# Optimization experiments

Hardware: AMD Instinct MI355X
Metric: run time of the kernel (lower is better)

Reference implementation:

```python
import jax, jax.numpy as jnp
import numpy as np

B_, D_, L_, N_ = 2, 1536, 2048, 16


def setup_inputs() -> dict:
    key = jax.random.key(0)
    ks = jax.random.split(key, 8)
    x = jax.random.normal(ks[0], (B_, D_, L_), dtype=jnp.float32)
    delta = jax.random.normal(ks[1], (B_, D_, L_), dtype=jnp.float32)
    # A negative (as in Mamba, A = -exp(A_log)) so the recurrence is stable
    A = -(jax.random.uniform(ks[2], (D_, N_), dtype=jnp.float32) + 0.5)
    B = jax.random.normal(ks[3], (B_, N_, L_), dtype=jnp.float32)
    C = jax.random.normal(ks[4], (B_, N_, L_), dtype=jnp.float32)
    D = jax.random.normal(ks[5], (D_,), dtype=jnp.float32)
    z = jax.random.normal(ks[6], (B_, D_, L_), dtype=jnp.float32)
    delta_bias = jax.random.normal(ks[7], (D_,), dtype=jnp.float32)
    return {"x": x, "delta": delta, "A": A, "B": B, "C": C,
            "D": D, "z": z, "delta_bias": delta_bias}


def reference(x, delta, A, B, C, D, z, delta_bias):
    # delta_softplus=True path with delta_bias, variable B (bnl) and C (bnl)
    delta = jax.nn.softplus(delta + delta_bias[None, :, None])      # (b,d,l)
    deltaA = jnp.exp(jnp.einsum('bdl,dn->bdln', delta, A))          # (b,d,l,n)
    deltaB_x = jnp.einsum('bdl,bnl,bdl->bdln', delta, B, x)         # (b,d,l,n)

    # scan over the sequence axis: h = deltaA_t * h + deltaB_x_t; y = h @ C_t
    dA_t = jnp.transpose(deltaA, (2, 0, 1, 3))     # (l,b,d,n)
    dBx_t = jnp.transpose(deltaB_x, (2, 0, 1, 3))  # (l,b,d,n)
    C_t = jnp.transpose(C, (2, 0, 1))              # (l,b,n)

    def step(h, inp):
        dA_i, dBx_i, C_i = inp
        h = dA_i * h + dBx_i                       # (b,d,n)
        y = jnp.einsum('bdn,bn->bd', h, C_i)       # (b,d)
        return h, y

    h0 = jnp.zeros((x.shape[0], A.shape[0], A.shape[1]), dtype=jnp.float32)
    _, ys = jax.lax.scan(step, h0, (dA_t, dBx_t, C_t))  # ys: (l,b,d)
    y = jnp.transpose(ys, (1, 2, 0))                    # (b,d,l)

    out = y + x * D[None, :, None]                      # D skip connection
    out = out * (z * jax.nn.sigmoid(z))                 # SiLU gate
    return out
```

## Files before the change

kernel.cpp:

```cpp
#include <hip/hip_runtime.h>
#include <math.h>

#define B_  2
#define D_  1536
#define L_  2048
#define N_  16
#define NH  8
#define LC  128
#define NCHUNK (L_ / LC)
#define NCH (B_ * D_)
#define LOG2E 1.4426950408889634f
#define LN2   0.6931471805599453f

typedef float f4 __attribute__((ext_vector_type(4)));
typedef float f8 __attribute__((ext_vector_type(8)));

__device__ __forceinline__ float exp2f_(float v) { return __builtin_amdgcn_exp2f(v); }
__device__ __forceinline__ float log2f_(float v) { return __builtin_amdgcn_logf(v); }
__device__ __forceinline__ float rcpf_(float v)  { return __builtin_amdgcn_rcpf(v); }

__device__ __forceinline__ float softplus_f(float v) {
    float t = exp2f_(v * LOG2E);
    float r = LN2 * log2f_(1.0f + t);
    return (v > 20.0f) ? v : r;
}
__device__ __forceinline__ f8 splat8(float v) { f8 r = {v,v,v,v,v,v,v,v}; return r; }
__device__ __forceinline__ f8 exp2v8(f8 a) {
    f8 r;
    r[0]=exp2f_(a[0]); r[1]=exp2f_(a[1]); r[2]=exp2f_(a[2]); r[3]=exp2f_(a[3]);
    r[4]=exp2f_(a[4]); r[5]=exp2f_(a[5]); r[6]=exp2f_(a[6]); r[7]=exp2f_(a[7]);
    return r;
}
__device__ __forceinline__ float dot8(f8 a, f8 b) {
    float p0 = fmaf(a[0], b[0], a[1]*b[1]);
    float p1 = fmaf(a[2], b[2], a[3]*b[3]);
    float p2 = fmaf(a[4], b[4], a[5]*b[5]);
    float p3 = fmaf(a[6], b[6], a[7]*b[7]);
    return (p0 + p1) + (p2 + p3);
}

#define DPP_ROW_SHR(N) (0x110 + (N))
#define DPP_ROW_BCAST15 0x142
#define DPP_WAVE_SHR1   0x138
template<int CTRL, int RMASK>
__device__ __forceinline__ float updpp(float old, float v) {
    return __int_as_float(__builtin_amdgcn_update_dpp(
        __float_as_int(old), __float_as_int(v), CTRL, RMASK, 0xF, false));
}

__global__ __launch_bounds__(64, 3)
void ssm_scan_kernel(const float* __restrict__ x,
                     const float* __restrict__ delta,
                     const float* __restrict__ A,
                     const float* __restrict__ Bm,
                     const float* __restrict__ Cm,
                     const float* __restrict__ Dv,
                     const float* __restrict__ z,
                     const float* __restrict__ dbias,
                     float* __restrict__ out)
{
    const int lane = threadIdx.x;
    const int s    = lane & 31;
    const int g    = lane >> 5;
    const int ch   = blockIdx.x;
    const int b    = ch / D_;
    const int d    = ch - b * D_;

    const float bias = dbias[d];
    const float Dd   = Dv[d];

    const float* Ab = A + d * N_ + NH * g;
    f8 A2v;
    A2v[0]=Ab[0]*LOG2E; A2v[1]=Ab[1]*LOG2E; A2v[2]=Ab[2]*LOG2E; A2v[3]=Ab[3]*LOG2E;
    A2v[4]=Ab[4]*LOG2E; A2v[5]=Ab[5]*LOG2E; A2v[6]=Ab[6]*LOG2E; A2v[7]=Ab[7]*LOG2E;

    const float* Bp = Bm + (size_t)b * (N_ * L_) + (size_t)(NH * g) * L_;
    const float* Cp = Cm + (size_t)b * (N_ * L_) + (size_t)(NH * g) * L_;
    const size_t chbase = (size_t)ch * L_;

    f8 carry = splat8(0.0f);

    for (int c = 0; c < NCHUNK; ++c) {
        const int off = c * LC + s * 4;

        f4 dv = *(const f4*)(delta + chbase + off);
        f4 xv = *(const f4*)(x     + chbase + off);
        f4 zv = *(const f4*)(z     + chbase + off);
#define LD_BC(i) f4 Bv##i = *(const f4*)(Bp + i * L_ + off); \
                 f4 Cv##i = *(const f4*)(Cp + i * L_ + off);
        LD_BC(0) LD_BC(1) LD_BC(2) LD_BC(3) LD_BC(4) LD_BC(5) LD_BC(6) LD_BC(7)

        float dt0 = softplus_f(dv.x + bias);
        float dt1 = softplus_f(dv.y + bias);
        float dt2 = softplus_f(dv.z + bias);
        float dt3 = softplus_f(dv.w + bias);
        float u0 = dt0 * xv.x, u1 = dt1 * xv.y, u2 = dt2 * xv.z, u3 = dt3 * xv.w;
        float dtsum = (dt0 + dt1) + (dt2 + dt3);

        f8 e0 = exp2v8(splat8(dt0) * A2v);
        f8 e1 = exp2v8(splat8(dt1) * A2v);
        f8 e2 = exp2v8(splat8(dt2) * A2v);
        f8 e3 = exp2v8(splat8(dt3) * A2v);
        f8 P  = exp2v8(splat8(dtsum) * A2v);

        f8 tB0 = {Bv0.x,Bv1.x,Bv2.x,Bv3.x,Bv4.x,Bv5.x,Bv6.x,Bv7.x};
        f8 tB1 = {Bv0.y,Bv1.y,Bv2.y,Bv3.y,Bv4.y,Bv5.y,Bv6.y,Bv7.y};
        f8 tB2 = {Bv0.z,Bv1.z,Bv2.z,Bv3.z,Bv4.z,Bv5.z,Bv6.z,Bv7.z};
        f8 tB3 = {Bv0.w,Bv1.w,Bv2.w,Bv3.w,Bv4.w,Bv5.w,Bv6.w,Bv7.w};
        f8 uB0 = splat8(u0) * tB0;
        f8 uB1 = splat8(u1) * tB1;
        f8 uB2 = splat8(u2) * tB2;
        f8 uB3 = splat8(u3) * tB3;
        f8 SC0 = {Cv0.x,Cv1.x,Cv2.x,Cv3.x,Cv4.x,Cv5.x,Cv6.x,Cv7.x};
        f8 SC1 = {Cv0.y,Cv1.y,Cv2.y,Cv3.y,Cv4.y,Cv5.y,Cv6.y,Cv7.y};
        f8 SC2 = {Cv0.z,Cv1.z,Cv2.z,Cv3.z,Cv4.z,Cv5.z,Cv6.z,Cv7.z};
        f8 SC3 = {Cv0.w,Cv1.w,Cv2.w,Cv3.w,Cv4.w,Cv5.w,Cv6.w,Cv7.w};

        f8 S = uB0;
        S = e1 * S + uB1;
        S = e2 * S + uB2;
        S = e3 * S + uB3;

#define SCAN_STEP(CTRL, RMASK) \
        { \
            _Pragma("unroll") \
            for (int i = 0; i < NH; ++i) { \
                float Pp = updpp<CTRL, RMASK>(1.0f, P[i]); \
                float Sp = updpp<CTRL, RMASK>(0.0f, S[i]); \
                S[i] = fmaf(Sp, P[i], S[i]);    \
                P[i] = P[i] * Pp; \
            } \
        }
        SCAN_STEP(DPP_ROW_SHR(1), 0xF)
        SCAN_STEP(DPP_ROW_SHR(2), 0xF)
        SCAN_STEP(DPP_ROW_SHR(4), 0xF)
        SCAN_STEP(DPP_ROW_SHR(8), 0xF)
        SCAN_STEP(DPP_ROW_BCAST15, 0xA)

        f8 h;
#pragma unroll
        for (int i = 0; i < NH; ++i) {
            float hinc = fmaf(carry[i], P[i], S[i]);
            float hup  = updpp<DPP_WAVE_SHR1, 0xF>(0.0f, hinc);
            h[i] = (s == 0) ? carry[i] : hup;
            carry[i] = __shfl(hinc, 31, 32);
        }

        h = e0 * h + uB0;  float y0 = dot8(h, SC0);
        h = e1 * h + uB1;  float y1 = dot8(h, SC1);
        h = e2 * h + uB2;  float y2 = dot8(h, SC2);
        h = e3 * h + uB3;  float y3 = dot8(h, SC3);

        y0 += __shfl_xor(y0, 32, 64);
        y1 += __shfl_xor(y1, 32, 64);
        y2 += __shfl_xor(y2, 32, 64);
        y3 += __shfl_xor(y3, 32, 64);
        if (g == 0) {
            float s0 = rcpf_(1.0f + exp2f_(-zv.x * LOG2E));
            float s1 = rcpf_(1.0f + exp2f_(-zv.y * LOG2E));
            float s2 = rcpf_(1.0f + exp2f_(-zv.z * LOG2E));
            float s3 = rcpf_(1.0f + exp2f_(-zv.w * LOG2E));
            f4 ov = { (y0 + xv.x * Dd) * (zv.x * s0),
                      (y1 + xv.y * Dd) * (zv.y * s1),
                      (y2 + xv.z * Dd) * (zv.z * s2),
                      (y3 + xv.w * Dd) * (zv.w * s3) };
            *(f4*)(out + chbase + off) = ov;
        }
    }
}

extern "C" void kernel_launch(void* const* d_in, const int* in_sizes, int n_in,
                              void* d_out, int out_size, void* d_ws, size_t ws_size,
                              hipStream_t stream) {
    const float* x     = (const float*)d_in[0];
    const float* delta = (const float*)d_in[1];
    const float* A     = (const float*)d_in[2];
    const float* Bm    = (const float*)d_in[3];
    const float* Cm    = (const float*)d_in[4];
    const float* Dv    = (const float*)d_in[5];
    const float* z     = (const float*)d_in[6];
    const float* dbias = (const float*)d_in[7];
    float* out = (float*)d_out;

    dim3 grid(NCH);
    dim3 block(64);
    ssm_scan_kernel<<<grid, block, 0, stream>>>(x, delta, A, Bm, Cm, Dv, z, dbias, out);
}
```

Measured before the change: 171.5 us.

## Prefetch next chunk inputs, compute P as product of exps, use readlane carry

Software-prefetches the next chunk's delta, x, z and B vectors into registers so their global loads overlap the current chunk's compute, and defers the C loads until after the local state is built. The chunk decay P is now the product of the four per-step exponentials instead of a fifth exp of the summed delta, which removes eight transcendental ops per lane per chunk. The state is reorganised per state index rather than per time step, avoiding the transposed f8 packs. The cross-chunk carry broadcast uses two scalar readlanes instead of a shuffle. Holding the prefetched vectors raises register pressure and may reduce occupancy.

```diff
diff --git a/kernel.cpp b/kernel.cpp
--- a/kernel.cpp
+++ b/kernel.cpp
@@ -24,19 +24,8 @@
     float r = LN2 * log2f_(1.0f + t);
     return (v > 20.0f) ? v : r;
 }
-__device__ __forceinline__ f8 splat8(float v) { f8 r = {v,v,v,v,v,v,v,v}; return r; }
-__device__ __forceinline__ f8 exp2v8(f8 a) {
-    f8 r;
-    r[0]=exp2f_(a[0]); r[1]=exp2f_(a[1]); r[2]=exp2f_(a[2]); r[3]=exp2f_(a[3]);
-    r[4]=exp2f_(a[4]); r[5]=exp2f_(a[5]); r[6]=exp2f_(a[6]); r[7]=exp2f_(a[7]);
-    return r;
-}
-__device__ __forceinline__ float dot8(f8 a, f8 b) {
-    float p0 = fmaf(a[0], b[0], a[1]*b[1]);
-    float p1 = fmaf(a[2], b[2], a[3]*b[3]);
-    float p2 = fmaf(a[4], b[4], a[5]*b[5]);
-    float p3 = fmaf(a[6], b[6], a[7]*b[7]);
-    return (p0 + p1) + (p2 + p3);
+__device__ __forceinline__ float rdlane(float v, int l) {
+    return __int_as_float(__builtin_amdgcn_readlane(__float_as_int(v), l));
 }
 
 #define DPP_ROW_SHR(N) (0x110 + (N))
@@ -70,56 +59,61 @@
     const float Dd   = Dv[d];
 
     const float* Ab = A + d * N_ + NH * g;
-    f8 A2v;
-    A2v[0]=Ab[0]*LOG2E; A2v[1]=Ab[1]*LOG2E; A2v[2]=Ab[2]*LOG2E; A2v[3]=Ab[3]*LOG2E;
-    A2v[4]=Ab[4]*LOG2E; A2v[5]=Ab[5]*LOG2E; A2v[6]=Ab[6]*LOG2E; A2v[7]=Ab[7]*LOG2E;
+    f8 A2;
+#pragma unroll
+    for (int i = 0; i < NH; ++i) A2[i] = Ab[i] * LOG2E;
 
     const float* Bp = Bm + (size_t)b * (N_ * L_) + (size_t)(NH * g) * L_;
     const float* Cp = Cm + (size_t)b * (N_ * L_) + (size_t)(NH * g) * L_;
     const size_t chbase = (size_t)ch * L_;
 
-    f8 carry = splat8(0.0f);
+    f8 carry = {0.0f,0.0f,0.0f,0.0f,0.0f,0.0f,0.0f,0.0f};
+
+    f4 pD = *(const f4*)(delta + chbase + s * 4);
+    f4 pX = *(const f4*)(x     + chbase + s * 4);
+    f4 pZ = *(const f4*)(z     + chbase + s * 4);
+#define PF_B(i) f4 pB##i = *(const f4*)(Bp + i * L_ + s * 4);
+    PF_B(0) PF_B(1) PF_B(2) PF_B(3) PF_B(4) PF_B(5) PF_B(6) PF_B(7)
 
     for (int c = 0; c < NCHUNK; ++c) {
-        const int off = c * LC + s * 4;
+        const int o = c * LC + s * 4;
 
-        f4 dv = *(const f4*)(delta + chbase + off);
-        f4 xv = *(const f4*)(x     + chbase + off);
-        f4 zv = *(const f4*)(z     + chbase + off);
-#define LD_BC(i) f4 Bv##i = *(const f4*)(Bp + i * L_ + off); \
-                 f4 Cv##i = *(const f4*)(Cp + i * L_ + off);
-        LD_BC(0) LD_BC(1) LD_BC(2) LD_BC(3) LD_BC(4) LD_BC(5) LD_BC(6) LD_BC(7)
+        f4 dv = pD, xv = pX, zv = pZ;
+#define CP_B(i) f4 B##i = pB##i;
+        CP_B(0) CP_B(1) CP_B(2) CP_B(3) CP_B(4) CP_B(5) CP_B(6) CP_B(7)
+
+        if (c + 1 < NCHUNK) {
+            const int o2 = o + LC;
+            pD = *(const f4*)(delta + chbase + o2);
+            pX = *(const f4*)(x     + chbase + o2);
+            pZ = *(const f4*)(z     + chbase + o2);
+#define PF_B2(i) pB##i = *(const f4*)(Bp + i * L_ + o2);
+            PF_B2(0) PF_B2(1) PF_B2(2) PF_B2(3) PF_B2(4) PF_B2(5) PF_B2(6) PF_B2(7)
+        }
 
         float dt0 = softplus_f(dv.x + bias);
         float dt1 = softplus_f(dv.y + bias);
         float dt2 = softplus_f(dv.z + bias);
         float dt3 = softplus_f(dv.w + bias);
-        float u0 = dt0 * xv.x, u1 = dt1 * xv.y, u2 = dt2 * xv.z, u3 = dt3 * xv.w;
-        float dtsum = (dt0 + dt1) + (dt2 + dt3);
+        f4 uv = { dt0 * xv.x, dt1 * xv.y, dt2 * xv.z, dt3 * xv.w };
 
-        f8 e0 = exp2v8(splat8(dt0) * A2v);
-        f8 e1 = exp2v8(splat8(dt1) * A2v);
-        f8 e2 = exp2v8(splat8(dt2) * A2v);
-        f8 e3 = exp2v8(splat8(dt3) * A2v);
-        f8 P  = exp2v8(splat8(dtsum) * A2v);
+        f8 S, P;
+#define STATE1(i) \
+        f4 e##i; \
+        e##i.x = exp2f_(dt0 * A2[i]); e##i.y = exp2f_(dt1 * A2[i]); \
+        e##i.z = exp2f_(dt2 * A2[i]); e##i.w = exp2f_(dt3 * A2[i]); \
+        f4 uB##i = uv * B##i; \
+        { float acc = uB##i.x; \
+          acc = fmaf(e##i.y, acc, uB##i.y); \
+          acc = fmaf(e##i.z, acc, uB##i.z); \
+          acc = fmaf(e##i.w, acc, uB##i.w); \
+          S[i] = acc; \
+          P[i] = (e##i.x * e##i.y) * (e##i.z * e##i.w); }
+        STATE1(0) STATE1(1) STATE1(2) STATE1(3)
+        STATE1(4) STATE1(5) STATE1(6) STATE1(7)
 
-        f8 tB0 = {Bv0.x,Bv1.x,Bv2.x,Bv3.x,Bv4.x,Bv5.x,Bv6.x,Bv7.x};
-        f8 tB1 = {Bv0.y,Bv1.y,Bv2.y,Bv3.y,Bv4.y,Bv5.y,Bv6.y,Bv7.y};
-        f8 tB2 = {Bv0.z,Bv1.z,Bv2.z,Bv3.z,Bv4.z,Bv5.z,Bv6.z,Bv7.z};
-        f8 tB3 = {Bv0.w,Bv1.w,Bv2.w,Bv3.w,Bv4.w,Bv5.w,Bv6.w,Bv7.w};
-        f8 uB0 = splat8(u0) * tB0;
-        f8 uB1 = splat8(u1) * tB1;
-        f8 uB2 = splat8(u2) * tB2;
-        f8 uB3 = splat8(u3) * tB3;
-        f8 SC0 = {Cv0.x,Cv1.x,Cv2.x,Cv3.x,Cv4.x,Cv5.x,Cv6.x,Cv7.x};
-        f8 SC1 = {Cv0.y,Cv1.y,Cv2.y,Cv3.y,Cv4.y,Cv5.y,Cv6.y,Cv7.y};
-        f8 SC2 = {Cv0.z,Cv1.z,Cv2.z,Cv3.z,Cv4.z,Cv5.z,Cv6.z,Cv7.z};
-        f8 SC3 = {Cv0.w,Cv1.w,Cv2.w,Cv3.w,Cv4.w,Cv5.w,Cv6.w,Cv7.w};
-
-        f8 S = uB0;
-        S = e1 * S + uB1;
-        S = e2 * S + uB2;
-        S = e3 * S + uB3;
+#define LD_C(i) f4 C##i = *(const f4*)(Cp + i * L_ + o);
+        LD_C(0) LD_C(1) LD_C(2) LD_C(3) LD_C(4) LD_C(5) LD_C(6) LD_C(7)
 
 #define SCAN_STEP(CTRL, RMASK) \
         { \
@@ -143,13 +137,19 @@
             float hinc = fmaf(carry[i], P[i], S[i]);
             float hup  = updpp<DPP_WAVE_SHR1, 0xF>(0.0f, hinc);
             h[i] = (s == 0) ? carry[i] : hup;
-            carry[i] = __shfl(hinc, 31, 32);
+            float c0 = rdlane(hinc, 31);
+            float c1 = rdlane(hinc, 63);
+            carry[i] = g ? c1 : c0;
         }
 
-        h = e0 * h + uB0;  float y0 = dot8(h, SC0);
-        h = e1 * h + uB1;  float y1 = dot8(h, SC1);
-        h = e2 * h + uB2;  float y2 = dot8(h, SC2);
-        h = e3 * h + uB3;  float y3 = dot8(h, SC3);
+        float y0 = 0.0f, y1 = 0.0f, y2 = 0.0f, y3 = 0.0f;
+#define STATE2(i) { float hh = h[i]; \
+        hh = fmaf(e##i.x, hh, uB##i.x); y0 = fmaf(hh, C##i.x, y0); \
+        hh = fmaf(e##i.y, hh, uB##i.y); y1 = fmaf(hh, C##i.y, y1); \
+        hh = fmaf(e##i.z, hh, uB##i.z); y2 = fmaf(hh, C##i.z, y2); \
+        hh = fmaf(e##i.w, hh, uB##i.w); y3 = fmaf(hh, C##i.w, y3); }
+        STATE2(0) STATE2(1) STATE2(2) STATE2(3)
+        STATE2(4) STATE2(5) STATE2(6) STATE2(7)
 
         y0 += __shfl_xor(y0, 32, 64);
         y1 += __shfl_xor(y1, 32, 64);
@@ -164,7 +164,7 @@
                       (y1 + xv.y * Dd) * (zv.y * s1),
                       (y2 + xv.z * Dd) * (zv.z * s2),
                       (y3 + xv.w * Dd) * (zv.w * s3) };
-            *(f4*)(out + chbase + off) = ov;
+            *(f4*)(out + chbase + o) = ov;
         }
     }
 }
```

Measured after the change: 303.6 us. 1.77x slower.
